# Performance work log

Measured on AMD Instinct MI355X. Metric: run time of the kernel, lower is better.

## Reference

```python
import jax, jax.numpy as jnp
import numpy as np
from functools import partial

B, T, F = 2048, 128, 64
H1, H2 = 512, 512


def _lstm(x, W, U, b, return_sequences):
    """Keras-semantics LSTM: gates order (i, f, c, o), recurrent_activation=sigmoid,
    cell activation=relu (as in activation='relu'). x: [B, T, F_in]."""
    Bs = x.shape[0]
    H = U.shape[0]
    # Precompute input contributions for all timesteps: [T, B, 4H]
    xg = (jnp.einsum('btf,fg->btg', x, W) + b).transpose(1, 0, 2)

    def step(carry, xt):
        h, c = carry
        g = xt + h @ U  # [B, 4H]
        i, f, cin, o = jnp.split(g, 4, axis=-1)
        i = jax.nn.sigmoid(i)
        f = jax.nn.sigmoid(f)
        o = jax.nn.sigmoid(o)
        c = f * c + i * jax.nn.relu(cin)
        h = o * jax.nn.relu(c)
        return (h, c), h

    h0 = jnp.zeros((Bs, H), dtype=x.dtype)
    c0 = jnp.zeros((Bs, H), dtype=x.dtype)
    (h, c), hs = jax.lax.scan(step, (h0, c0), xg)
    if return_sequences:
        return hs.transpose(1, 0, 2)  # [B, T, H]
    return h  # [B, H]


def setup_inputs() -> dict:
    key = jax.random.key(0)
    ks = jax.random.split(key, 9)
    s = 0.02  # small init so the relu cell stays numerically tame
    return {
        'x':  jax.random.normal(ks[0], (B, T, F), dtype=jnp.float32),
        'W1': jax.random.normal(ks[1], (F, 4 * H1), dtype=jnp.float32) * s,
        'U1': jax.random.normal(ks[2], (H1, 4 * H1), dtype=jnp.float32) * s,
        'b1': jnp.zeros((4 * H1,), dtype=jnp.float32),
        'W2': jax.random.normal(ks[3], (H1, 4 * H2), dtype=jnp.float32) * s,
        'U2': jax.random.normal(ks[4], (H2, 4 * H2), dtype=jnp.float32) * s,
        'b2': jnp.zeros((4 * H2,), dtype=jnp.float32),
        'Wd': jax.random.normal(ks[5], (H2, 1), dtype=jnp.float32) * s,
        'bd': jnp.zeros((1,), dtype=jnp.float32),
    }


def reference(x, W1, U1, b1, W2, U2, b2, Wd, bd):
    h1 = _lstm(x, W1, U1, b1, return_sequences=True)   # [B, T, H1]
    h2 = _lstm(h1, W2, U2, b2, return_sequences=False)  # [B, H2]
    return h2 @ Wd + bd  # [B, 1]
```

## Files before the change

kernel.cpp:

```cpp
#include <hip/hip_runtime.h>

#define TT   128
#define FF   64
#define HH   512
#define GG   2048
#define K1   576
#define K2   1024
#define KB1  72
#define KB2  128
#define NBLK 256
#define QS   520

using f16x8 = __attribute__((ext_vector_type(8))) _Float16;
using f16x4 = __attribute__((ext_vector_type(4))) _Float16;
using f16x2 = __attribute__((ext_vector_type(2))) _Float16;
using f32x4 = __attribute__((ext_vector_type(4))) float;

__global__ void pack_weights(const float* __restrict__ U, const float* __restrict__ W,
                             const float* __restrict__ bias, int K8, int Kh,
                             _Float16* __restrict__ Bp, float* __restrict__ pb)
{
    __shared__ _Float16 T[8][GG];
    const int kb = blockIdx.x;
    const int tid = threadIdx.x;
    for (int i = tid; i < 8 * (GG / 4); i += 256) {
        int r = i / (GG / 4), c4 = (i % (GG / 4)) * 4;
        int k = kb * 8 + r;
        const float* src = (k < Kh) ? (U + (size_t)k * GG) : (W + (size_t)(k - Kh) * GG);
        float4 v = *(const float4*)(src + c4);
        T[r][c4 + 0] = (_Float16)v.x; T[r][c4 + 1] = (_Float16)v.y;
        T[r][c4 + 2] = (_Float16)v.z; T[r][c4 + 3] = (_Float16)v.w;
    }
    __syncthreads();
    for (int m = tid; m < 2048; m += 256) {
        int ct = m >> 4, c = m & 15;
        int col = (c & 3) * HH + ct * 4 + (c >> 2);
        f16x8 v;
#pragma unroll
        for (int j = 0; j < 8; ++j) v[j] = T[j][col];
        *(f16x8*)(Bp + (((size_t)ct * K8 + kb) * 16 + c) * 8) = v;
    }
    if (kb == 0)
        for (int p = tid; p < GG; p += 256) {
            int ct = p >> 4, c = p & 15;
            pb[p] = bias[(c & 3) * HH + ct * 4 + (c >> 2)];
        }
}

template <int CTRL>
__device__ __forceinline__ float qbcast(float v) {
    return __int_as_float(__builtin_amdgcn_mov_dpp(__float_as_int(v), CTRL, 0xF, 0xF, true));
}

__device__ __forceinline__ void gld_lds16_sc0(const _Float16* g, _Float16* l) {
    __builtin_amdgcn_global_load_lds(
        (__attribute__((address_space(1))) const void*)g,
        (__attribute__((address_space(3))) void*)l, 16, 0, 1);
}

__device__ __forceinline__ void lstm_epi(
    f32x4 v4, float bias, float* __restrict__ cs, _Float16* __restrict__ hstp,
    int R0, int kq, int c, int ubase)
{
    const int gsel = c & 3;
    const int ub = ubase + (c >> 2);
#pragma unroll
    for (int j = 0; j < 4; ++j) {
        float v = v4[j] + bias;
        float sig = 1.f / (1.f + __expf(-v));
        float act = (gsel == 2) ? (v > 0.f ? v : 0.f) : sig;
        float ig  = qbcast<0x00>(act);
        float fg  = qbcast<0x55>(act);
        float cin = qbcast<0xAA>(act);
        float og  = qbcast<0xFF>(act);
        int Rl = kq * 4 + j;
        int R = R0 + Rl;
        float cp = cs[R * 33 + ub];
        float cn = fg * cp + ig * cin;
        float hn = og * (cn > 0.f ? cn : 0.f);
        if (gsel == 0) {
            cs[R * 33 + ub] = cn;
            hstp[Rl * 40 + ub] = (_Float16)hn;
        }
    }
}

#define MFMA16(av, bv, acc) \
    acc = __builtin_amdgcn_mfma_f32_16x16x32_f16(av, bv, acc, 0, 0, 0)

__global__ __launch_bounds__(512, 2) void lstm_persist(
    const float* __restrict__ x,
    const _Float16* __restrict__ Bp1, const float* __restrict__ pb1,
    const _Float16* __restrict__ Bp2, const float* __restrict__ pb2,
    const float* __restrict__ Wd, const float* __restrict__ bd,
    _Float16* __restrict__ h1b,
    _Float16* __restrict__ h2b,
    unsigned* __restrict__ bar,
    float* __restrict__ out)
{
    __shared__ _Float16 Q1[2][16 * QS];
    __shared__ _Float16 Q2[2][16 * QS];
    __shared__ _Float16 Xp[2][16][72];
    __shared__ float    c1s[128 * 33];
    __shared__ float    c2s[128 * 33];
    __shared__ _Float16 hst[2][2][16][40];

    const int tid = threadIdx.x;
    const int w = tid >> 6, lane = tid & 63;
    const int b = blockIdx.x;
    const int rg = 2 * (b & 7) + ((b >> 3) & 1);
    const int cg = b >> 4;
    const int r0 = rg * 128;
    const int c = lane & 15, kq = lane >> 4;

    for (int i = tid; i < 128 * 33; i += 512) { c1s[i] = 0.f; c2s[i] = 0.f; }
    for (int i = tid; i < 2 * 2 * 16 * 40; i += 512) (&hst[0][0][0][0])[i] = (_Float16)0.f;

    const int ct = cg * 8 + w;
    f16x8 w1f[18], w2f[32];
#pragma unroll
    for (int kc = 0; kc < 18; ++kc)
        w1f[kc] = *(const f16x8*)(Bp1 + (((size_t)ct * KB1 + kc * 4 + kq) * 16 + c) * 8);
#pragma unroll
    for (int kc = 0; kc < 32; ++kc)
        w2f[kc] = *(const f16x8*)(Bp2 + (((size_t)ct * KB2 + kc * 4 + kq) * 16 + c) * 8);
#pragma unroll
    for (int kc = 0; kc < 18; ++kc) asm volatile("" : "+a"(w1f[kc]));
#pragma unroll
    for (int kc = 0; kc < 32; ++kc) asm volatile("" : "+a"(w2f[kc]));

    const float bias1 = pb1[ct * 16 + c];
    const float bias2 = pb2[ct * 16 + c];
    const int ub0 = w * 4;

    const int xrow = tid >> 5, xc2 = (tid & 31) * 2;

    for (int s = 0; s <= TT; ++s) {
        const int pr1 = (s + 1) & 1, pw1 = s & 1;
        const int pr2 = s & 1,       pw2 = (s + 1) & 1;
        const _Float16* h1r = h1b + (size_t)pr1 * 2048 * HH;
        const _Float16* h2r = h2b + (size_t)pr2 * 2048 * HH;
        _Float16* h1w = h1b + (size_t)pw1 * 2048 * HH;
        _Float16* h2w = h2b + (size_t)pw2 * 2048 * HH;
        const bool notLast = (s < TT);

        {
#pragma unroll
            for (int i = 0; i < 2; ++i) {
                int r = w * 2 + i;
                gld_lds16_sc0(h1r + (size_t)(r0 + r) * HH + lane * 8, &Q1[0][r * QS]);
                gld_lds16_sc0(h2r + (size_t)(r0 + r) * HH + lane * 8, &Q2[0][r * QS]);
            }
            if (notLast) {
                float2 xv = *(const float2*)(x + ((size_t)(r0 + xrow) * TT + s) * FF + xc2);
                *(f16x2*)&Xp[0][xrow][xc2] = (f16x2){(_Float16)xv.x, (_Float16)xv.y};
            }
        }
        __syncthreads();

        for (int ch = 0; ch <= 8; ++ch) {
            const int par = ch & 1;

            if (ch <= 6) {
                const int gr = r0 + (ch + 1) * 16;
#pragma unroll
                for (int i = 0; i < 2; ++i) {
                    int r = w * 2 + i;
                    gld_lds16_sc0(h1r + (size_t)(gr + r) * HH + lane * 8, &Q1[par ^ 1][r * QS]);
                    gld_lds16_sc0(h2r + (size_t)(gr + r) * HH + lane * 8, &Q2[par ^ 1][r * QS]);
                }
            }
            float2 xnext{0.f, 0.f};
            const bool havex = (ch <= 6) && notLast;
            if (havex)
                xnext = *(const float2*)(x +
                    ((size_t)(r0 + (ch + 1) * 16 + xrow) * TT + s) * FF + xc2);

            if (ch >= 1 && tid < 256) {
                int layer = tid >> 7, r = (tid >> 3) & 15, cq = tid & 7;
                f16x4 hv = *(const f16x4*)&hst[par ^ 1][layer][r][cq * 4];
                _Float16* dst = (layer ? h2w : h1w)
                    + (size_t)(r0 + (ch - 1) * 16 + r) * HH + cg * 32 + cq * 4;
                *(f16x4*)dst = hv;
            }

            if (ch <= 7) {
                const char* q1b = (const char*)&Q1[par][0] + c * (QS * 2);
                const char* q2b = (const char*)&Q2[par][0] + c * (QS * 2);
                if (notLast) {
                    f32x4 a0{0.f, 0.f, 0.f, 0.f}, a1 = a0;
#pragma unroll
                    for (int kc = 0; kc < 8; ++kc) {
                        f16x8 av = *(const f16x8*)(q1b + kc * 64 + kq * 16);
                        MFMA16(av, w1f[kc], a0);
                    }
#pragma unroll
                    for (int kc = 8; kc < 16; ++kc) {
                        f16x8 av = *(const f16x8*)(q1b + kc * 64 + kq * 16);
                        MFMA16(av, w1f[kc], a1);
                    }
                    {
                        f16x8 av = *(const f16x8*)&Xp[par][c][kq * 8];
                        MFMA16(av, w1f[16], a0);
                        av = *(const f16x8*)&Xp[par][c][32 + kq * 8];
                        MFMA16(av, w1f[17], a1);
                    }
                    lstm_epi(a0 + a1, bias1, c1s, &hst[par][0][0][0], ch * 16, kq, c, ub0);
                }
                if (s >= 1) {
                    f32x4 b0{0.f, 0.f, 0.f, 0.f}, b1 = b0;
#pragma unroll
                    for (int kc = 0; kc < 16; ++kc) {
                        f16x8 av = *(const f16x8*)(q2b + kc * 64 + kq * 16);
                        MFMA16(av, w2f[kc], b0);
                    }
#pragma unroll
                    for (int kc = 0; kc < 16; ++kc) {
                        f16x8 av = *(const f16x8*)(q1b + kc * 64 + kq * 16);
                        MFMA16(av, w2f[16 + kc], b1);
                    }
                    lstm_epi(b0 + b1, bias2, c2s, &hst[par][1][0][0], ch * 16, kq, c, ub0);
                }
            }

            if (havex)
                *(f16x2*)&Xp[par ^ 1][xrow][xc2] =
                    (f16x2){(_Float16)xnext.x, (_Float16)xnext.y};

            __syncthreads();
        }

        if (tid == 0) {
            __hip_atomic_fetch_add(&bar[rg * 32], 1u,
                                   __ATOMIC_RELAXED, __HIP_MEMORY_SCOPE_AGENT);
            const unsigned target = 16u * (unsigned)(s + 1);
            while (__hip_atomic_load(&bar[rg * 32],
                                     __ATOMIC_RELAXED, __HIP_MEMORY_SCOPE_AGENT) < target)
                __builtin_amdgcn_s_sleep(2);
        }
        __syncthreads();
    }

    if (cg == 0) {
        const _Float16* hf = h2b + (size_t)((TT + 1) & 1) * 2048 * HH;
        int row = tid >> 2, part = tid & 3;
        const _Float16* hr = hf + (size_t)(r0 + row) * HH + part * 128;
        const float* wd = Wd + part * 128;
        float ssum = 0.f;
#pragma unroll
        for (int u8 = 0; u8 < 16; ++u8) {
            f16x8 hv = *(const f16x8*)(hr + u8 * 8);
#pragma unroll
            for (int k = 0; k < 8; ++k) ssum += (float)hv[k] * wd[u8 * 8 + k];
        }
        ssum += __shfl_xor(ssum, 1);
        ssum += __shfl_xor(ssum, 2);
        if (part == 0) out[r0 + row] = ssum + bd[0];
    }
}

extern "C" void kernel_launch(void* const* d_in, const int* in_sizes, int n_in,
                              void* d_out, int out_size, void* d_ws, size_t ws_size,
                              hipStream_t stream)
{
    const float* x  = (const float*)d_in[0];
    const float* W1 = (const float*)d_in[1];
    const float* U1 = (const float*)d_in[2];
    const float* b1 = (const float*)d_in[3];
    const float* W2 = (const float*)d_in[4];
    const float* U2 = (const float*)d_in[5];
    const float* b2 = (const float*)d_in[6];
    const float* Wd = (const float*)d_in[7];
    const float* bd = (const float*)d_in[8];
    float* out = (float*)d_out;

    char* ws = (char*)d_ws;
    size_t off = 0;
    _Float16* Bp1 = (_Float16*)(ws + off); off += (size_t)K1 * GG * 2;
    _Float16* Bp2 = (_Float16*)(ws + off); off += (size_t)K2 * GG * 2;
    float*    pb1 = (float*)(ws + off);    off += (size_t)GG * 4;
    float*    pb2 = (float*)(ws + off);    off += (size_t)GG * 4;
    _Float16* h1b = (_Float16*)(ws + off); off += (size_t)2 * 2048 * HH * 2;
    _Float16* h2b = (_Float16*)(ws + off); off += (size_t)2 * 2048 * HH * 2;
    unsigned* bar = (unsigned*)(ws + off); off += 16 * 32 * 4;

    hipMemsetAsync(h1b, 0, (size_t)2 * 2048 * HH * 2, stream);
    hipMemsetAsync(h2b, 0, (size_t)2 * 2048 * HH * 2, stream);
    hipMemsetAsync(bar, 0, 16 * 32 * 4, stream);

    pack_weights<<<KB1, 256, 0, stream>>>(U1, W1, b1, KB1, HH, Bp1, pb1);
    pack_weights<<<KB2, 256, 0, stream>>>(U2, W2, b2, KB2, HH, Bp2, pb2);
    lstm_persist<<<NBLK, 512, 0, stream>>>(x, Bp1, pb1, Bp2, pb2, Wd, bd,
                                           h1b, h2b, bar, out);
}
```

Measured before the change: 4.556 ms.

## Split K across wave pairs so each A fragment feeds two gate tiles

Each wave now computes two column tiles over half of the K dimension. Every LDS A-fragment load therefore feeds two MFMAs, which halves the LDS read traffic per MFMA. Partial sums are exchanged through a new shared buffer, and the LSTM epilogue is deferred by one chunk so the exchange rides on the existing barrier. The extra pipeline stage adds an epilogue-flush chunk and a tail writeback with an extra barrier, plus more shared memory that could lower occupancy.

```diff
diff --git a/kernel.cpp b/kernel.cpp
--- a/kernel.cpp
+++ b/kernel.cpp
@@ -104,9 +104,11 @@
     __shared__ float    c1s[128 * 33];
     __shared__ float    c2s[128 * 33];
     __shared__ _Float16 hst[2][2][16][40];
+    __shared__ float    xb[2][2][4][2][256];
 
     const int tid = threadIdx.x;
     const int w = tid >> 6, lane = tid & 63;
+    const int p = w & 3, kh = w >> 2;
     const int b = blockIdx.x;
     const int rg = 2 * (b & 7) + ((b >> 3) & 1);
     const int cg = b >> 4;
@@ -116,22 +118,30 @@
     for (int i = tid; i < 128 * 33; i += 512) { c1s[i] = 0.f; c2s[i] = 0.f; }
     for (int i = tid; i < 2 * 2 * 16 * 40; i += 512) (&hst[0][0][0][0])[i] = (_Float16)0.f;
 
-    const int ct = cg * 8 + w;
-    f16x8 w1f[18], w2f[32];
-#pragma unroll
-    for (int kc = 0; kc < 18; ++kc)
-        w1f[kc] = *(const f16x8*)(Bp1 + (((size_t)ct * KB1 + kc * 4 + kq) * 16 + c) * 8);
-#pragma unroll
-    for (int kc = 0; kc < 32; ++kc)
-        w2f[kc] = *(const f16x8*)(Bp2 + (((size_t)ct * KB2 + kc * 4 + kq) * 16 + c) * 8);
-#pragma unroll
-    for (int kc = 0; kc < 18; ++kc) asm volatile("" : "+a"(w1f[kc]));
-#pragma unroll
-    for (int kc = 0; kc < 32; ++kc) asm volatile("" : "+a"(w2f[kc]));
-
-    const float bias1 = pb1[ct * 16 + c];
-    const float bias2 = pb2[ct * 16 + c];
-    const int ub0 = w * 4;
+    const int ct0 = cg * 8 + 2 * p;
+    f16x8 w1f[2][9], w2f[2][16];
+#pragma unroll
+    for (int ti = 0; ti < 2; ++ti) {
+#pragma unroll
+        for (int kc = 0; kc < 9; ++kc)
+            w1f[ti][kc] = *(const f16x8*)(Bp1 +
+                (((size_t)(ct0 + ti) * KB1 + (kh * 9 + kc) * 4 + kq) * 16 + c) * 8);
+#pragma unroll
+        for (int kc = 0; kc < 16; ++kc)
+            w2f[ti][kc] = *(const f16x8*)(Bp2 +
+                (((size_t)(ct0 + ti) * KB2 + (kh * 16 + kc) * 4 + kq) * 16 + c) * 8);
+    }
+#pragma unroll
+    for (int ti = 0; ti < 2; ++ti) {
+#pragma unroll
+        for (int kc = 0; kc < 9; ++kc) asm volatile("" : "+a"(w1f[ti][kc]));
+#pragma unroll
+        for (int kc = 0; kc < 16; ++kc) asm volatile("" : "+a"(w2f[ti][kc]));
+    }
+
+    const float bias1 = pb1[(ct0 + kh) * 16 + c];
+    const float bias2 = pb2[(ct0 + kh) * 16 + c];
+    const int ub0 = (2 * p + kh) * 4;
 
     const int xrow = tid >> 5, xc2 = (tid & 31) * 2;
 
@@ -158,6 +168,8 @@
         }
         __syncthreads();
 
+        f32x4 ownA{0.f, 0.f, 0.f, 0.f}, ownB = ownA;
+
         for (int ch = 0; ch <= 8; ++ch) {
             const int par = ch & 1;
 
@@ -176,12 +188,24 @@
                 xnext = *(const float2*)(x +
                     ((size_t)(r0 + (ch + 1) * 16 + xrow) * TT + s) * FF + xc2);
 
-            if (ch >= 1 && tid < 256) {
+            if (ch >= 2 && tid < 256) {
                 int layer = tid >> 7, r = (tid >> 3) & 15, cq = tid & 7;
-                f16x4 hv = *(const f16x4*)&hst[par ^ 1][layer][r][cq * 4];
+                f16x4 hv = *(const f16x4*)&hst[par][layer][r][cq * 4];
                 _Float16* dst = (layer ? h2w : h1w)
-                    + (size_t)(r0 + (ch - 1) * 16 + r) * HH + cg * 32 + cq * 4;
+                    + (size_t)(r0 + (ch - 2) * 16 + r) * HH + cg * 32 + cq * 4;
                 *(f16x4*)dst = hv;
+            }
+
+            if (ch >= 1) {
+                const int R0 = (ch - 1) * 16;
+                if (notLast) {
+                    f32x4 f = ownA + *(const f32x4*)&xb[par ^ 1][0][p][kh ^ 1][lane * 4];
+                    lstm_epi(f, bias1, c1s, &hst[par ^ 1][0][0][0], R0, kq, c, ub0);
+                }
+                if (s >= 1) {
+                    f32x4 f = ownB + *(const f32x4*)&xb[par ^ 1][1][p][kh ^ 1][lane * 4];
+                    lstm_epi(f, bias2, c2s, &hst[par ^ 1][1][0][0], R0, kq, c, ub0);
+                }
             }
 
             if (ch <= 7) {
@@ -189,37 +213,42 @@
                 const char* q2b = (const char*)&Q2[par][0] + c * (QS * 2);
                 if (notLast) {
                     f32x4 a0{0.f, 0.f, 0.f, 0.f}, a1 = a0;
-#pragma unroll
-                    for (int kc = 0; kc < 8; ++kc) {
-                        f16x8 av = *(const f16x8*)(q1b + kc * 64 + kq * 16);
-                        MFMA16(av, w1f[kc], a0);
+                    if (kh == 0) {
+#pragma unroll
+                        for (int kc = 0; kc < 9; ++kc) {
+                            f16x8 av = *(const f16x8*)(q1b + kc * 64 + kq * 16);
+                            MFMA16(av, w1f[0][kc], a0); MFMA16(av, w1f[1][kc], a1);
+                        }
+                    } else {
+#pragma unroll
+                        for (int kc = 0; kc < 7; ++kc) {
+                            f16x8 av = *(const f16x8*)(q1b + (kc + 9) * 64 + kq * 16);
+                            MFMA16(av, w1f[0][kc], a0); MFMA16(av, w1f[1][kc], a1);
+                        }
+                        {
+                            f16x8 av = *(const f16x8*)&Xp[par][c][kq * 8];
+                            MFMA16(av, w1f[0][7], a0); MFMA16(av, w1f[1][7], a1);
+                            av = *(const f16x8*)&Xp[par][c][32 + kq * 8];
+                            MFMA16(av, w1f[0][8], a0); MFMA16(av, w1f[1][8], a1);
+                        }
                     }
-#pragma unroll
-                    for (int kc = 8; kc < 16; ++kc) {
-                        f16x8 av = *(const f16x8*)(q1b + kc * 64 + kq * 16);
-                        MFMA16(av, w1f[kc], a1);
+                    f32x4 mine   = (kh == 0) ? a0 : a1;
+                    f32x4 theirs = (kh == 0) ? a1 : a0;
+                    *(f32x4*)&xb[par][0][p][kh][lane * 4] = theirs;
+                    ownA = mine;
+                }
+                if (s >= 1) {
+                    const char* qb = kh ? q1b : q2b;
+                    f32x4 b0{0.f, 0.f, 0.f, 0.f}, b1 = b0;
+#pragma unroll
+                    for (int kc = 0; kc < 16; ++kc) {
+                        f16x8 av = *(const f16x8*)(qb + kc * 64 + kq * 16);
+                        MFMA16(av, w2f[0][kc], b0); MFMA16(av, w2f[1][kc], b1);
                     }
-                    {
-                        f16x8 av = *(const f16x8*)&Xp[par][c][kq * 8];
-                        MFMA16(av, w1f[16], a0);
-                        av = *(const f16x8*)&Xp[par][c][32 + kq * 8];
-                        MFMA16(av, w1f[17], a1);
-                    }
-                    lstm_epi(a0 + a1, bias1, c1s, &hst[par][0][0][0], ch * 16, kq, c, ub0);
-                }
-                if (s >= 1) {
-                    f32x4 b0{0.f, 0.f, 0.f, 0.f}, b1 = b0;
-#pragma unroll
-                    for (int kc = 0; kc < 16; ++kc) {
-                        f16x8 av = *(const f16x8*)(q2b + kc * 64 + kq * 16);
-                        MFMA16(av, w2f[kc], b0);
-                    }
-#pragma unroll
-                    for (int kc = 0; kc < 16; ++kc) {
-                        f16x8 av = *(const f16x8*)(q1b + kc * 64 + kq * 16);
-                        MFMA16(av, w2f[16 + kc], b1);
-                    }
-                    lstm_epi(b0 + b1, bias2, c2s, &hst[par][1][0][0], ch * 16, kq, c, ub0);
+                    f32x4 mine   = (kh == 0) ? b0 : b1;
+                    f32x4 theirs = (kh == 0) ? b1 : b0;
+                    *(f32x4*)&xb[par][1][p][kh][lane * 4] = theirs;
+                    ownB = mine;
                 }
             }
 
@@ -229,6 +258,15 @@
 
             __syncthreads();
         }
+
+        if (tid < 256) {
+            int layer = tid >> 7, r = (tid >> 3) & 15, cq = tid & 7;
+            f16x4 hv = *(const f16x4*)&hst[1][layer][r][cq * 4];
+            _Float16* dst = (layer ? h2w : h1w)
+                + (size_t)(r0 + 112 + r) * HH + cg * 32 + cq * 4;
+            *(f16x4*)dst = hv;
+        }
+        __syncthreads();
 
         if (tid == 0) {
             __hip_atomic_fetch_add(&bar[rg * 32], 1u,
```

Result: slower. 4.699 ms (+3.1%).

## Replace per-timestep group barrier with per-chunk progress counters for fine-grained sync

Applied to the files above, without the earlier changes.

Flattens the timestep×chunk double loop into one linear chunk stream and replaces the per-timestep atomic barrier across the 16 column-group blocks with per-block progress counters. Before loading or writing a chunk, each block waits until every peer's counter is past a lag threshold. This lets blocks drift by a few chunks instead of stalling at every timestep boundary. It also splits the layer-2 accumulation into four independent MFMA chains to shorten the dependency chain. The risk is a race if the lag thresholds are too loose, plus extra polling traffic every chunk.

```diff
diff --git a/kernel.cpp b/kernel.cpp
--- a/kernel.cpp
+++ b/kernel.cpp
@@ -10,6 +10,7 @@
 #define KB2  128
 #define NBLK 256
 #define QS   520
+#define NCH  1032
 
 using f16x8 = __attribute__((ext_vector_type(8))) _Float16;
 using f16x4 = __attribute__((ext_vector_type(4))) _Float16;
@@ -58,6 +59,17 @@
         (__attribute__((address_space(3))) void*)l, 16, 0, 1);
 }
 
+__device__ __forceinline__ void wait_min_ge(const unsigned* slots, int lane, int target) {
+    if (target <= 0) return;
+    for (;;) {
+        unsigned v = 0xFFFFFFFFu;
+        if (lane < 16)
+            v = __hip_atomic_load(slots + lane, __ATOMIC_RELAXED, __HIP_MEMORY_SCOPE_AGENT);
+        if (__all(v >= (unsigned)target)) break;
+        __builtin_amdgcn_s_sleep(1);
+    }
+}
+
 __device__ __forceinline__ void lstm_epi(
     f32x4 v4, float bias, float* __restrict__ cs, _Float16* __restrict__ hstp,
     int R0, int kq, int c, int ubase)
@@ -73,14 +85,13 @@
         float fg  = qbcast<0x55>(act);
         float cin = qbcast<0xAA>(act);
         float og  = qbcast<0xFF>(act);
-        int Rl = kq * 4 + j;
-        int R = R0 + Rl;
+        int R = R0 + kq * 4 + j;
         float cp = cs[R * 33 + ub];
         float cn = fg * cp + ig * cin;
         float hn = og * (cn > 0.f ? cn : 0.f);
         if (gsel == 0) {
             cs[R * 33 + ub] = cn;
-            hstp[Rl * 40 + ub] = (_Float16)hn;
+            hstp[(kq * 4 + j) * 40 + ub] = (_Float16)hn;
         }
     }
 }
@@ -95,7 +106,8 @@
     const float* __restrict__ Wd, const float* __restrict__ bd,
     _Float16* __restrict__ h1b,
     _Float16* __restrict__ h2b,
-    unsigned* __restrict__ bar,
+    unsigned* __restrict__ progb,
+    unsigned* __restrict__ fbar,
     float* __restrict__ out)
 {
     __shared__ _Float16 Q1[2][16 * QS];
@@ -113,6 +125,8 @@
     const int r0 = rg * 128;
     const int c = lane & 15, kq = lane >> 4;
 
+    unsigned* prog = progb + rg * 16;
+
     for (int i = tid; i < 128 * 33; i += 512) { c1s[i] = 0.f; c2s[i] = 0.f; }
     for (int i = tid; i < 2 * 2 * 16 * 40; i += 512) (&hst[0][0][0][0])[i] = (_Float16)0.f;
 
@@ -132,114 +146,120 @@
     const float bias1 = pb1[ct * 16 + c];
     const float bias2 = pb2[ct * 16 + c];
     const int ub0 = w * 4;
-
     const int xrow = tid >> 5, xc2 = (tid & 31) * 2;
 
-    for (int s = 0; s <= TT; ++s) {
-        const int pr1 = (s + 1) & 1, pw1 = s & 1;
-        const int pr2 = s & 1,       pw2 = (s + 1) & 1;
-        const _Float16* h1r = h1b + (size_t)pr1 * 2048 * HH;
-        const _Float16* h2r = h2b + (size_t)pr2 * 2048 * HH;
-        _Float16* h1w = h1b + (size_t)pw1 * 2048 * HH;
-        _Float16* h2w = h2b + (size_t)pw2 * 2048 * HH;
-        const bool notLast = (s < TT);
-
-        {
+    {
+#pragma unroll
+        for (int i = 0; i < 2; ++i) {
+            int r = w * 2 + i;
+            gld_lds16_sc0(h1b + (size_t)1 * 2048 * HH + (size_t)(r0 + r) * HH + lane * 8,
+                          &Q1[0][r * QS]);
+            gld_lds16_sc0(h2b + (size_t)(r0 + r) * HH + lane * 8, &Q2[0][r * QS]);
+        }
+        float2 xv = *(const float2*)(x + ((size_t)(r0 + xrow) * TT + 0) * FF + xc2);
+        *(f16x2*)&Xp[0][xrow][xc2] = (f16x2){(_Float16)xv.x, (_Float16)xv.y};
+    }
+    __syncthreads();
+
+    for (int it = 0; it <= NCH; ++it) {
+        const int par = it & 1;
+
+        if (tid == 0)
+            __hip_atomic_store(&prog[cg], (unsigned)(it + 1),
+                               __ATOMIC_RELAXED, __HIP_MEMORY_SCOPE_AGENT);
+
+        if (it <= NCH - 2) {
+            const int k = it + 1, sk = k >> 3, ck = k & 7;
+            if (k >= 8) wait_min_ge(prog, lane, it - 4);
+            const _Float16* h1r = h1b + (size_t)((sk + 1) & 1) * 2048 * HH;
+            const _Float16* h2r = h2b + (size_t)(sk & 1) * 2048 * HH;
+            const int gr = r0 + ck * 16;
 #pragma unroll
             for (int i = 0; i < 2; ++i) {
                 int r = w * 2 + i;
-                gld_lds16_sc0(h1r + (size_t)(r0 + r) * HH + lane * 8, &Q1[0][r * QS]);
-                gld_lds16_sc0(h2r + (size_t)(r0 + r) * HH + lane * 8, &Q2[0][r * QS]);
+                gld_lds16_sc0(h1r + (size_t)(gr + r) * HH + lane * 8, &Q1[par ^ 1][r * QS]);
+                gld_lds16_sc0(h2r + (size_t)(gr + r) * HH + lane * 8, &Q2[par ^ 1][r * QS]);
             }
-            if (notLast) {
-                float2 xv = *(const float2*)(x + ((size_t)(r0 + xrow) * TT + s) * FF + xc2);
-                *(f16x2*)&Xp[0][xrow][xc2] = (f16x2){(_Float16)xv.x, (_Float16)xv.y};
+            if (sk < TT) {
+                float2 xv = *(const float2*)(x + ((size_t)(gr + xrow) * TT + sk) * FF + xc2);
+                *(f16x2*)&Xp[par ^ 1][xrow][xc2] = (f16x2){(_Float16)xv.x, (_Float16)xv.y};
             }
         }
+
+        if (it >= 1 && tid < 256) {
+            const int k2 = it - 1, s2 = k2 >> 3, c2 = k2 & 7;
+            if (k2 >= 8) wait_min_ge(prog, lane, it - 8);
+            _Float16* h1w = h1b + (size_t)(s2 & 1) * 2048 * HH;
+            _Float16* h2w = h2b + (size_t)((s2 + 1) & 1) * 2048 * HH;
+            int layer = tid >> 7, r = (tid >> 3) & 15, cq = tid & 7;
+            f16x4 hv = *(const f16x4*)&hst[par ^ 1][layer][r][cq * 4];
+            _Float16* dst = (layer ? h2w : h1w)
+                + (size_t)(r0 + c2 * 16 + r) * HH + cg * 32 + cq * 4;
+            *(f16x4*)dst = hv;
+        }
+
+        if (it <= NCH - 1) {
+            const int s = it >> 3;
+            const int R0 = (it & 7) * 16;
+            const char* q1b = (const char*)&Q1[par][0] + c * (QS * 2);
+            const char* q2b = (const char*)&Q2[par][0] + c * (QS * 2);
+            if (s < TT) {
+                f32x4 a0{0.f, 0.f, 0.f, 0.f}, a1 = a0;
+#pragma unroll
+                for (int kc = 0; kc < 8; ++kc) {
+                    f16x8 av = *(const f16x8*)(q1b + kc * 64 + kq * 16);
+                    MFMA16(av, w1f[kc], a0);
+                }
+#pragma unroll
+                for (int kc = 8; kc < 16; ++kc) {
+                    f16x8 av = *(const f16x8*)(q1b + kc * 64 + kq * 16);
+                    MFMA16(av, w1f[kc], a1);
+                }
+                {
+                    f16x8 av = *(const f16x8*)&Xp[par][c][kq * 8];
+                    MFMA16(av, w1f[16], a0);
+                    av = *(const f16x8*)&Xp[par][c][32 + kq * 8];
+                    MFMA16(av, w1f[17], a1);
+                }
+                lstm_epi(a0 + a1, bias1, c1s, &hst[par][0][0][0], R0, kq, c, ub0);
+            }
+            if (s >= 1) {
+                f32x4 b0{0.f, 0.f, 0.f, 0.f}, b1 = b0, b2 = b0, b3 = b0;
+#pragma unroll
+                for (int kc = 0; kc < 8; ++kc) {
+                    f16x8 av = *(const f16x8*)(q2b + kc * 64 + kq * 16);
+                    MFMA16(av, w2f[kc], b0);
+                }
+#pragma unroll
+                for (int kc = 8; kc < 16; ++kc) {
+                    f16x8 av = *(const f16x8*)(q2b + kc * 64 + kq * 16);
+                    MFMA16(av, w2f[kc], b1);
+                }
+#pragma unroll
+                for (int kc = 0; kc < 8; ++kc) {
+                    f16x8 av = *(const f16x8*)(q1b + kc * 64 + kq * 16);
+                    MFMA16(av, w2f[16 + kc], b2);
+                }
+#pragma unroll
+                for (int kc = 8; kc < 16; ++kc) {
+                    f16x8 av = *(const f16x8*)(q1b + kc * 64 + kq * 16);
+                    MFMA16(av, w2f[16 + kc], b3);
+                }
+                lstm_epi((b0 + b1) + (b2 + b3), bias2, c2s, &hst[par][1][0][0], R0, kq, c, ub0);
+            }
+        }
+
         __syncthreads();
-
-        for (int ch = 0; ch <= 8; ++ch) {
-            const int par = ch & 1;
-
-            if (ch <= 6) {
-                const int gr = r0 + (ch + 1) * 16;
-#pragma unroll
-                for (int i = 0; i < 2; ++i) {
-                    int r = w * 2 + i;
-                    gld_lds16_sc0(h1r + (size_t)(gr + r) * HH + lane * 8, &Q1[par ^ 1][r * QS]);
-                    gld_lds16_sc0(h2r + (size_t)(gr + r) * HH + lane * 8, &Q2[par ^ 1][r * QS]);
-                }
-            }
-            float2 xnext{0.f, 0.f};
-            const bool havex = (ch <= 6) && notLast;
-            if (havex)
-                xnext = *(const float2*)(x +
-                    ((size_t)(r0 + (ch + 1) * 16 + xrow) * TT + s) * FF + xc2);
-
-            if (ch >= 1 && tid < 256) {
-                int layer = tid >> 7, r = (tid >> 3) & 15, cq = tid & 7;
-                f16x4 hv = *(const f16x4*)&hst[par ^ 1][layer][r][cq * 4];
-                _Float16* dst = (layer ? h2w : h1w)
-                    + (size_t)(r0 + (ch - 1) * 16 + r) * HH + cg * 32 + cq * 4;
-                *(f16x4*)dst = hv;
-            }
-
-            if (ch <= 7) {
-                const char* q1b = (const char*)&Q1[par][0] + c * (QS * 2);
-                const char* q2b = (const char*)&Q2[par][0] + c * (QS * 2);
-                if (notLast) {
-                    f32x4 a0{0.f, 0.f, 0.f, 0.f}, a1 = a0;
-#pragma unroll
-                    for (int kc = 0; kc < 8; ++kc) {
-                        f16x8 av = *(const f16x8*)(q1b + kc * 64 + kq * 16);
-                        MFMA16(av, w1f[kc], a0);
-                    }
-#pragma unroll
-                    for (int kc = 8; kc < 16; ++kc) {
-                        f16x8 av = *(const f16x8*)(q1b + kc * 64 + kq * 16);
-                        MFMA16(av, w1f[kc], a1);
-                    }
-                    {
-                        f16x8 av = *(const f16x8*)&Xp[par][c][kq * 8];
-                        MFMA16(av, w1f[16], a0);
-                        av = *(const f16x8*)&Xp[par][c][32 + kq * 8];
-                        MFMA16(av, w1f[17], a1);
-                    }
-                    lstm_epi(a0 + a1, bias1, c1s, &hst[par][0][0][0], ch * 16, kq, c, ub0);
-                }
-                if (s >= 1) {
-                    f32x4 b0{0.f, 0.f, 0.f, 0.f}, b1 = b0;
-#pragma unroll
-                    for (int kc = 0; kc < 16; ++kc) {
-                        f16x8 av = *(const f16x8*)(q2b + kc * 64 + kq * 16);
-                        MFMA16(av, w2f[kc], b0);
-                    }
-#pragma unroll
-                    for (int kc = 0; kc < 16; ++kc) {
-                        f16x8 av = *(const f16x8*)(q1b + kc * 64 + kq * 16);
-                        MFMA16(av, w2f[16 + kc], b1);
-                    }
-                    lstm_epi(b0 + b1, bias2, c2s, &hst[par][1][0][0], ch * 16, kq, c, ub0);
-                }
-            }
-
-            if (havex)
-                *(f16x2*)&Xp[par ^ 1][xrow][xc2] =
-                    (f16x2){(_Float16)xnext.x, (_Float16)xnext.y};
-
-            __syncthreads();
-        }
-
-        if (tid == 0) {
-            __hip_atomic_fetch_add(&bar[rg * 32], 1u,
-                                   __ATOMIC_RELAXED, __HIP_MEMORY_SCOPE_AGENT);
-            const unsigned target = 16u * (unsigned)(s + 1);
-            while (__hip_atomic_load(&bar[rg * 32],
-                                     __ATOMIC_RELAXED, __HIP_MEMORY_SCOPE_AGENT) < target)
-                __builtin_amdgcn_s_sleep(2);
-        }
-        __syncthreads();
-    }
+    }
+
+    if (tid == 0) {
+        __hip_atomic_fetch_add(&fbar[rg * 32], 1u,
+                               __ATOMIC_RELAXED, __HIP_MEMORY_SCOPE_AGENT);
+        while (__hip_atomic_load(&fbar[rg * 32],
+                                 __ATOMIC_RELAXED, __HIP_MEMORY_SCOPE_AGENT) < 16u)
+            __builtin_amdgcn_s_sleep(2);
+    }
+    __syncthreads();
 
     if (cg == 0) {
         const _Float16* hf = h2b + (size_t)((TT + 1) & 1) * 2048 * HH;
@@ -282,14 +302,15 @@
     float*    pb2 = (float*)(ws + off);    off += (size_t)GG * 4;
     _Float16* h1b = (_Float16*)(ws + off); off += (size_t)2 * 2048 * HH * 2;
     _Float16* h2b = (_Float16*)(ws + off); off += (size_t)2 * 2048 * HH * 2;
-    unsigned* bar = (unsigned*)(ws + off); off += 16 * 32 * 4;
+    unsigned* prg = (unsigned*)(ws + off); off += 16 * 16 * 4;
+    unsigned* fbr = (unsigned*)(ws + off); off += 16 * 32 * 4;
 
     hipMemsetAsync(h1b, 0, (size_t)2 * 2048 * HH * 2, stream);
     hipMemsetAsync(h2b, 0, (size_t)2 * 2048 * HH * 2, stream);
-    hipMemsetAsync(bar, 0, 16 * 32 * 4, stream);
+    hipMemsetAsync(prg, 0, 16 * 16 * 4 + 16 * 32 * 4, stream);
 
     pack_weights<<<KB1, 256, 0, stream>>>(U1, W1, b1, KB1, HH, Bp1, pb1);
     pack_weights<<<KB2, 256, 0, stream>>>(U2, W2, b2, KB2, HH, Bp2, pb2);
     lstm_persist<<<NBLK, 512, 0, stream>>>(x, Bp1, pb1, Bp2, pb2, Wd, bd,
-                                           h1b, h2b, bar, out);
-}
+                                           h1b, h2b, prg, fbr, out);
+}
```

Result: slower. 5.449 ms (+19.6%).
